# Kernel optimization log

Measured on AMD Instinct MI355X. Metric: run time of the kernel, lower is better.

Reference implementation:

```python
import jax, jax.numpy as jnp
import numpy as np

SEQ, BATCH = 2048, 32
ENC_HS, DEC_HS = 512, 1024

def setup_inputs() -> dict:
    key = jax.random.key(0)
    k1, k2, k3, k4, k5 = jax.random.split(key, 5)
    return {
        "hidden": jax.random.normal(k1, (BATCH, DEC_HS), dtype=jnp.float32),
        "encoder_outputs": jax.random.normal(k2, (SEQ, BATCH, 2 * ENC_HS), dtype=jnp.float32),
        "attn_w": jax.random.normal(k3, (2 * ENC_HS + DEC_HS, DEC_HS), dtype=jnp.float32) * 0.02,
        "attn_b": jax.random.normal(k4, (DEC_HS,), dtype=jnp.float32) * 0.02,
        "v": jax.random.normal(k5, (DEC_HS,), dtype=jnp.float32),
    }

def reference(hidden, encoder_outputs, attn_w, attn_b, v):
    # encoder_outputs: [S, B, 2*enc_hs] -> [B, S, 2*enc_hs]
    enc = jnp.transpose(encoder_outputs, (1, 0, 2))
    B, S, _ = enc.shape
    # hidden: [B, dec_hs] broadcast to [B, S, dec_hs]
    h = jnp.broadcast_to(hidden[:, None, :], (B, S, hidden.shape[-1]))
    cat = jnp.concatenate([h, enc], axis=2)            # [B, S, 2*enc_hs+dec_hs]
    energy = jnp.tanh(cat @ attn_w + attn_b)            # [B, S, dec_hs]
    scores = jnp.einsum("bsd,d->bs", energy, v)        # [B, S]
    return jax.nn.softmax(scores, axis=1)
```

## Files before the change

### kernel.cpp

```cpp
#include <hip/hip_runtime.h>


typedef _Float16 f16;
typedef _Float16 half8 __attribute__((ext_vector_type(8)));
typedef float f32x4 __attribute__((ext_vector_type(4)));

#define KDIM 1024
#define NDIM 1024
#define SEQ  2048
#define NB   32

typedef __attribute__((address_space(1))) void gvoid;
typedef __attribute__((address_space(3))) void svoid;

__device__ __forceinline__ void gload_lds16(const void* g, void* l) {
    __builtin_amdgcn_global_load_lds((const gvoid*)g, (svoid*)l, 16, 0, 0);
}

__global__ __launch_bounds__(256) void prep_w(const float* __restrict__ w,
                                              f16* __restrict__ wt) {
    int idx   = blockIdx.x * 256 + threadIdx.x;
    int t     = idx >> 11;
    int unit  = idx & 2047;
    int nloc  = unit >> 2;
    int kblk  = unit & 3;
    int kstep = t >> 1, npass = t & 1;
    int n_g   = npass * 512 + nloc;
    int kbase = kstep * 32 + kblk * 8;
    half8 h;
#pragma unroll
    for (int kk = 0; kk < 8; ++kk)
        h[kk] = (f16)w[(size_t)(1024 + kbase + kk) * 1024 + n_g];
    int p = nloc * 4 + ((kblk + (nloc >> 1)) & 3);
    *(half8*)&wt[(size_t)t * 16384 + p * 8] = h;
}

__global__ __launch_bounds__(256) void prep_hb(const float* __restrict__ hidden,
                                               const float* __restrict__ attn_w,
                                               const float* __restrict__ attn_b,
                                               float* __restrict__ hb) {
    int b = blockIdx.x >> 2;
    int n = (blockIdx.x & 3) * 256 + threadIdx.x;
    const float* h = hidden + (size_t)b * 1024;
    float acc = attn_b[n];
#pragma unroll 8
    for (int k = 0; k < 1024; ++k)
        acc += h[k] * attn_w[(size_t)k * 1024 + n];
    hb[(size_t)b * 1024 + n] = acc;
}

__global__ __launch_bounds__(512, 2)
void fused_energy(const float* __restrict__ enc, const f16* __restrict__ wt,
                  const float* __restrict__ hb, const float* __restrict__ vvec,
                  float* __restrict__ out) {
    __shared__ f16 As[128 * 32];
    __shared__ f16 Ws[512 * 32];
    __shared__ float red[4][128];

    const int tid  = threadIdx.x;
    const int lane = tid & 63;
    const int wv   = tid >> 6;
    const int wm   = wv >> 2;
    const int wn   = wv & 3;
    const int l15  = lane & 15;
    const int l4   = lane >> 4;
    const int wgrow = blockIdx.x * 128;

    const int ar  = tid >> 2;
    const int akb = tid & 3;
    const float* aG = enc + (size_t)(wgrow + ar) * KDIM + akb * 8;
    f16* aDst = &As[(ar * 4 + ((akb + (ar >> 1)) & 3)) * 8];

    const int wseg = wv * 4;
    char* wLds = (char*)Ws + wseg * 1024 + lane * 16;

    int aOff[4], bOff[8];
#pragma unroll
    for (int mi = 0; mi < 4; ++mi) {
        int r = wm * 64 + mi * 16 + l15;
        aOff[mi] = (r * 4 + ((l4 + (r >> 1)) & 3)) * 8;
    }
#pragma unroll
    for (int nj = 0; nj < 8; ++nj) {
        int n = wn * 128 + nj * 16 + l15;
        bOff[nj] = (n * 4 + ((l4 + (n >> 1)) & 3)) * 8;
    }

    float part[4][4];
#pragma unroll
    for (int mi = 0; mi < 4; ++mi)
#pragma unroll
        for (int rg = 0; rg < 4; ++rg) part[mi][rg] = 0.f;

    const f32x4 zero = {0.f, 0.f, 0.f, 0.f};

    for (int pass = 0; pass < 2; ++pass) {
        f32x4 acc[4][8];
#pragma unroll
        for (int mi = 0; mi < 4; ++mi)
#pragma unroll
            for (int nj = 0; nj < 8; ++nj) acc[mi][nj] = zero;

        for (int ks = 0; ks < 32; ++ks) {
            f32x4 a0 = *(const f32x4*)(aG + ks * 32);
            f32x4 a1 = *(const f32x4*)(aG + ks * 32 + 4);
            __syncthreads();
            {
                const char* wsrc = (const char*)wt +
                    (size_t)(ks * 2 + pass) * 32768 + wseg * 1024 + lane * 16;
#pragma unroll
                for (int i = 0; i < 4; ++i)
                    gload_lds16(wsrc + i * 1024, wLds + i * 1024);
            }
            half8 ah;
#pragma unroll
            for (int j = 0; j < 4; ++j) ah[j] = (f16)a0[j];
#pragma unroll
            for (int j = 0; j < 4; ++j) ah[4 + j] = (f16)a1[j];
            *(half8*)aDst = ah;
            __syncthreads();

            half8 bf[8];
#pragma unroll
            for (int nj = 0; nj < 8; ++nj) bf[nj] = *(const half8*)&Ws[bOff[nj]];
#pragma unroll
            for (int mi = 0; mi < 4; ++mi) {
                half8 af = *(const half8*)&As[aOff[mi]];
#pragma unroll
                for (int nj = 0; nj < 8; ++nj)
                    acc[mi][nj] = __builtin_amdgcn_mfma_f32_16x16x32_f16(
                        af, bf[nj], acc[mi][nj], 0, 0, 0);
            }
        }

        const int nbase = pass * 512 + wn * 128;
        float vv[8];
#pragma unroll
        for (int nj = 0; nj < 8; ++nj) vv[nj] = vvec[nbase + nj * 16 + l15];
#pragma unroll
        for (int mi = 0; mi < 4; ++mi) {
#pragma unroll
            for (int rg = 0; rg < 4; ++rg) {
                int rl = wm * 64 + mi * 16 + l4 * 4 + rg;
                const float* hbrow = hb + (size_t)(rl & 31) * NDIM + nbase + l15;
                float sum = 0.f;
#pragma unroll
                for (int nj = 0; nj < 8; ++nj) {
                    float e  = acc[mi][nj][rg] + hbrow[nj * 16];
                    float e2 = __expf(2.f * e);
                    float th = 1.f - 2.f / (e2 + 1.f);
                    sum += th * vv[nj];
                }
                part[mi][rg] += sum;
            }
        }
    }

#pragma unroll
    for (int mi = 0; mi < 4; ++mi) {
#pragma unroll
        for (int rg = 0; rg < 4; ++rg) {
            float p = part[mi][rg];
            p += __shfl_xor(p, 1);
            p += __shfl_xor(p, 2);
            p += __shfl_xor(p, 4);
            p += __shfl_xor(p, 8);
            if (l15 == 0) red[wn][wm * 64 + mi * 16 + l4 * 4 + rg] = p;
        }
    }
    __syncthreads();
    if (tid < 128) {
        float s = red[0][tid] + red[1][tid] + red[2][tid] + red[3][tid];
        int rG = wgrow + tid;
        out[(size_t)(rG & 31) * SEQ + (rG >> 5)] = s;
    }
}

__global__ __launch_bounds__(256) void softmax_rows(float* __restrict__ out) {
    const int b = blockIdx.x;
    float* row = out + (size_t)b * SEQ;
    const int tid  = threadIdx.x;
    const int lane = tid & 63;
    const int wv   = tid >> 6;
    __shared__ float sred[4];
    __shared__ float ssum[4];
    float x[8];
    float mx = -3.4e38f;
#pragma unroll
    for (int j = 0; j < 8; ++j) { x[j] = row[tid + j * 256]; mx = fmaxf(mx, x[j]); }
#pragma unroll
    for (int o = 1; o < 64; o <<= 1) mx = fmaxf(mx, __shfl_xor(mx, o));
    if (lane == 0) sred[wv] = mx;
    __syncthreads();
    mx = fmaxf(fmaxf(sred[0], sred[1]), fmaxf(sred[2], sred[3]));
    float s = 0.f;
#pragma unroll
    for (int j = 0; j < 8; ++j) { x[j] = __expf(x[j] - mx); s += x[j]; }
#pragma unroll
    for (int o = 1; o < 64; o <<= 1) s += __shfl_xor(s, o);
    if (lane == 0) ssum[wv] = s;
    __syncthreads();
    s = ssum[0] + ssum[1] + ssum[2] + ssum[3];
    float inv = 1.f / s;
#pragma unroll
    for (int j = 0; j < 8; ++j) row[tid + j * 256] = x[j] * inv;
}

extern "C" void kernel_launch(void* const* d_in, const int* in_sizes, int n_in,
                              void* d_out, int out_size, void* d_ws, size_t ws_size,
                              hipStream_t stream) {
    const float* hidden = (const float*)d_in[0];
    const float* enc    = (const float*)d_in[1];
    const float* attn_w = (const float*)d_in[2];
    const float* attn_b = (const float*)d_in[3];
    const float* v      = (const float*)d_in[4];
    float* out = (float*)d_out;

    f16*   wt = (f16*)d_ws;
    float* hb = (float*)((char*)d_ws + (2u << 20));

    prep_w<<<512, 256, 0, stream>>>(attn_w, wt);
    prep_hb<<<128, 256, 0, stream>>>(hidden, attn_w, attn_b, hb);
    fused_energy<<<512, 512, 0, stream>>>(enc, wt, hb, v, out);
    softmax_rows<<<32, 256, 0, stream>>>(out);
}
```

Baseline: 284.9 us.

## Double-buffer LDS tiles to prefetch next K-step during MFMA compute

Splits the A and W shared-memory tiles into two buffers. The next K-step's weights (via global_load_lds) and encoder rows are prefetched while MFMAs run on the current buffer, and the loop drops to a single barrier per iteration. The prefetch runs continuously across the two N passes. This aims to hide global load latency and remove one barrier per step, at the cost of doubling LDS use, which may cut the number of resident blocks per CU.

```diff
diff --git a/kernel.cpp b/kernel.cpp
--- a/kernel.cpp
+++ b/kernel.cpp
@@ -53,8 +53,8 @@
 void fused_energy(const float* __restrict__ enc, const f16* __restrict__ wt,
                   const float* __restrict__ hb, const float* __restrict__ vvec,
                   float* __restrict__ out) {
-    __shared__ f16 As[128 * 32];
-    __shared__ f16 Ws[512 * 32];
+    __shared__ f16 As[2][128 * 32];
+    __shared__ f16 Ws[2][512 * 32];
     __shared__ float red[4][128];
 
     const int tid  = threadIdx.x;
@@ -69,10 +69,10 @@
     const int ar  = tid >> 2;
     const int akb = tid & 3;
     const float* aG = enc + (size_t)(wgrow + ar) * KDIM + akb * 8;
-    f16* aDst = &As[(ar * 4 + ((akb + (ar >> 1)) & 3)) * 8];
+    const int aDstOff = (ar * 4 + ((akb + (ar >> 1)) & 3)) * 8;
 
     const int wseg = wv * 4;
-    char* wLds = (char*)Ws + wseg * 1024 + lane * 16;
+    const int wLdsOff = wseg * 1024 + lane * 16;
 
     int aOff[4], bOff[8];
 #pragma unroll
@@ -94,6 +94,21 @@
 
     const f32x4 zero = {0.f, 0.f, 0.f, 0.f};
 
+    {
+        const char* wsrc = (const char*)wt + wLdsOff;
+        char* wd = (char*)&Ws[0][0] + wLdsOff;
+#pragma unroll
+        for (int i = 0; i < 4; ++i)
+            gload_lds16(wsrc + i * 1024, wd + i * 1024);
+        f32x4 a0 = *(const f32x4*)(aG);
+        f32x4 a1 = *(const f32x4*)(aG + 4);
+        half8 ah;
+#pragma unroll
+        for (int j = 0; j < 4; ++j) { ah[j] = (f16)a0[j]; ah[4 + j] = (f16)a1[j]; }
+        *(half8*)&As[0][aDstOff] = ah;
+    }
+    __syncthreads();
+
     for (int pass = 0; pass < 2; ++pass) {
         f32x4 acc[4][8];
 #pragma unroll
@@ -101,36 +116,46 @@
 #pragma unroll
             for (int nj = 0; nj < 8; ++nj) acc[mi][nj] = zero;
 
+#pragma unroll 2
         for (int ks = 0; ks < 32; ++ks) {
-            f32x4 a0 = *(const f32x4*)(aG + ks * 32);
-            f32x4 a1 = *(const f32x4*)(aG + ks * 32 + 4);
-            __syncthreads();
-            {
+            const int cur = ks & 1;
+            const int nxb = cur ^ 1;
+            const int tn  = pass * 32 + ks + 1;
+            const bool pf = tn < 64;
+            const int nks = tn & 31;
+            const int nps = tn >> 5;
+
+            f32x4 a0, a1;
+            if (pf) {
                 const char* wsrc = (const char*)wt +
-                    (size_t)(ks * 2 + pass) * 32768 + wseg * 1024 + lane * 16;
+                    (size_t)(nks * 2 + nps) * 32768 + wLdsOff;
+                char* wd = (char*)&Ws[nxb][0] + wLdsOff;
 #pragma unroll
                 for (int i = 0; i < 4; ++i)
-                    gload_lds16(wsrc + i * 1024, wLds + i * 1024);
-            }
-            half8 ah;
-#pragma unroll
-            for (int j = 0; j < 4; ++j) ah[j] = (f16)a0[j];
-#pragma unroll
-            for (int j = 0; j < 4; ++j) ah[4 + j] = (f16)a1[j];
-            *(half8*)aDst = ah;
-            __syncthreads();
+                    gload_lds16(wsrc + i * 1024, wd + i * 1024);
+                a0 = *(const f32x4*)(aG + nks * 32);
+                a1 = *(const f32x4*)(aG + nks * 32 + 4);
+            }
 
             half8 bf[8];
 #pragma unroll
-            for (int nj = 0; nj < 8; ++nj) bf[nj] = *(const half8*)&Ws[bOff[nj]];
+            for (int nj = 0; nj < 8; ++nj) bf[nj] = *(const half8*)&Ws[cur][bOff[nj]];
 #pragma unroll
             for (int mi = 0; mi < 4; ++mi) {
-                half8 af = *(const half8*)&As[aOff[mi]];
+                half8 af = *(const half8*)&As[cur][aOff[mi]];
 #pragma unroll
                 for (int nj = 0; nj < 8; ++nj)
                     acc[mi][nj] = __builtin_amdgcn_mfma_f32_16x16x32_f16(
                         af, bf[nj], acc[mi][nj], 0, 0, 0);
             }
+
+            if (pf) {
+                half8 ah;
+#pragma unroll
+                for (int j = 0; j < 4; ++j) { ah[j] = (f16)a0[j]; ah[4 + j] = (f16)a1[j]; }
+                *(half8*)&As[nxb][aDstOff] = ah;
+            }
+            __syncthreads();
         }
 
         const int nbase = pass * 512 + wn * 128;
```

Result: faster. 269.4 us (-5.5%).

## Triple-buffer W and A tiles in LDS with one barrier per k-step

Applied to the files above, without the earlier changes.

Restructures the fused energy GEMM main loop into a 3-stage software pipeline. W tiles are loaded asynchronously into LDS two steps ahead, and A rows are prefetched into registers and converted to f16 one step ahead. This replaces the two __syncthreads per k-step with a single barrier and explicit vmcnt waits, so global loads overlap with the MFMA work. The cost is 3x the LDS footprint (about 123KB), which may limit occupancy with launch_bounds(512,2), and added reliance on hand-written waitcnt correctness.

```diff
diff --git a/kernel.cpp b/kernel.cpp
--- a/kernel.cpp
+++ b/kernel.cpp
@@ -53,8 +53,8 @@
 void fused_energy(const float* __restrict__ enc, const f16* __restrict__ wt,
                   const float* __restrict__ hb, const float* __restrict__ vvec,
                   float* __restrict__ out) {
-    __shared__ f16 As[128 * 32];
-    __shared__ f16 Ws[512 * 32];
+    __shared__ f16 Ws[3][512 * 32];
+    __shared__ f16 As[3][128 * 32];
     __shared__ float red[4][128];
 
     const int tid  = threadIdx.x;
@@ -69,21 +69,20 @@
     const int ar  = tid >> 2;
     const int akb = tid & 3;
     const float* aG = enc + (size_t)(wgrow + ar) * KDIM + akb * 8;
-    f16* aDst = &As[(ar * 4 + ((akb + (ar >> 1)) & 3)) * 8];
-
-    const int wseg = wv * 4;
-    char* wLds = (char*)Ws + wseg * 1024 + lane * 16;
-
-    int aOff[4], bOff[8];
+    const int aDstByte = (ar * 4 + ((akb + (ar >> 1)) & 3)) * 16;
+
+    const int wLdsOff = wv * 4096 + lane * 16;
+
+    int aOffB[4], bOffB[8];
 #pragma unroll
     for (int mi = 0; mi < 4; ++mi) {
         int r = wm * 64 + mi * 16 + l15;
-        aOff[mi] = (r * 4 + ((l4 + (r >> 1)) & 3)) * 8;
+        aOffB[mi] = (r * 4 + ((l4 + (r >> 1)) & 3)) * 16;
     }
 #pragma unroll
     for (int nj = 0; nj < 8; ++nj) {
         int n = wn * 128 + nj * 16 + l15;
-        bOff[nj] = (n * 4 + ((l4 + (n >> 1)) & 3)) * 8;
+        bOffB[nj] = (n * 4 + ((l4 + (n >> 1)) & 3)) * 16;
     }
 
     float part[4][4];
@@ -93,68 +92,119 @@
         for (int rg = 0; rg < 4; ++rg) part[mi][rg] = 0.f;
 
     const f32x4 zero = {0.f, 0.f, 0.f, 0.f};
-
-    for (int pass = 0; pass < 2; ++pass) {
-        f32x4 acc[4][8];
-#pragma unroll
-        for (int mi = 0; mi < 4; ++mi)
-#pragma unroll
-            for (int nj = 0; nj < 8; ++nj) acc[mi][nj] = zero;
-
-        for (int ks = 0; ks < 32; ++ks) {
-            f32x4 a0 = *(const f32x4*)(aG + ks * 32);
-            f32x4 a1 = *(const f32x4*)(aG + ks * 32 + 4);
-            __syncthreads();
-            {
-                const char* wsrc = (const char*)wt +
-                    (size_t)(ks * 2 + pass) * 32768 + wseg * 1024 + lane * 16;
-#pragma unroll
-                for (int i = 0; i < 4; ++i)
-                    gload_lds16(wsrc + i * 1024, wLds + i * 1024);
-            }
-            half8 ah;
-#pragma unroll
-            for (int j = 0; j < 4; ++j) ah[j] = (f16)a0[j];
-#pragma unroll
-            for (int j = 0; j < 4; ++j) ah[4 + j] = (f16)a1[j];
-            *(half8*)aDst = ah;
-            __syncthreads();
-
-            half8 bf[8];
-#pragma unroll
-            for (int nj = 0; nj < 8; ++nj) bf[nj] = *(const half8*)&Ws[bOff[nj]];
-#pragma unroll
-            for (int mi = 0; mi < 4; ++mi) {
-                half8 af = *(const half8*)&As[aOff[mi]];
-#pragma unroll
-                for (int nj = 0; nj < 8; ++nj)
-                    acc[mi][nj] = __builtin_amdgcn_mfma_f32_16x16x32_f16(
-                        af, bf[nj], acc[mi][nj], 0, 0, 0);
-            }
-        }
-
-        const int nbase = pass * 512 + wn * 128;
-        float vv[8];
-#pragma unroll
-        for (int nj = 0; nj < 8; ++nj) vv[nj] = vvec[nbase + nj * 16 + l15];
-#pragma unroll
-        for (int mi = 0; mi < 4; ++mi) {
-#pragma unroll
-            for (int rg = 0; rg < 4; ++rg) {
-                int rl = wm * 64 + mi * 16 + l4 * 4 + rg;
-                const float* hbrow = hb + (size_t)(rl & 31) * NDIM + nbase + l15;
-                float sum = 0.f;
-#pragma unroll
-                for (int nj = 0; nj < 8; ++nj) {
-                    float e  = acc[mi][nj][rg] + hbrow[nj * 16];
-                    float e2 = __expf(2.f * e);
-                    float th = 1.f - 2.f / (e2 + 1.f);
-                    sum += th * vv[nj];
-                }
-                part[mi][rg] += sum;
-            }
-        }
-    }
+    f32x4 acc[4][8];
+#pragma unroll
+    for (int mi = 0; mi < 4; ++mi)
+#pragma unroll
+        for (int nj = 0; nj < 8; ++nj) acc[mi][nj] = zero;
+
+    f32x4 aEv0, aEv1, aOd0, aOd1;
+
+    {
+        const char* w0 = (const char*)wt + wLdsOff;
+        char* d0 = (char*)&Ws[0][0] + wLdsOff;
+        gload_lds16(w0,        d0);
+        gload_lds16(w0 + 1024, d0 + 1024);
+        gload_lds16(w0 + 2048, d0 + 2048);
+        gload_lds16(w0 + 3072, d0 + 3072);
+        aEv0 = *(const f32x4*)aG;
+        aEv1 = *(const f32x4*)(aG + 4);
+        const char* w1 = (const char*)wt + (size_t)2 * 32768 + wLdsOff;
+        char* d1 = (char*)&Ws[1][0] + wLdsOff;
+        gload_lds16(w1,        d1);
+        gload_lds16(w1 + 1024, d1 + 1024);
+        gload_lds16(w1 + 2048, d1 + 2048);
+        gload_lds16(w1 + 3072, d1 + 3072);
+        aOd0 = *(const f32x4*)(aG + 32);
+        aOd1 = *(const f32x4*)(aG + 36);
+        asm volatile("s_waitcnt vmcnt(6)" ::: "memory");
+        half8 ah;
+#pragma unroll
+        for (int j = 0; j < 4; ++j) { ah[j] = (f16)aEv0[j]; ah[4 + j] = (f16)aEv1[j]; }
+        *(half8*)((char*)&As[0][0] + aDstByte) = ah;
+    }
+    asm volatile("s_waitcnt lgkmcnt(0)" ::: "memory");
+    __builtin_amdgcn_s_barrier();
+
+#define KSTEP(T, ALD0, ALD1, ACV0, ACV1)                                      \
+  {                                                                           \
+    const int t_ = (T);                                                       \
+    if (t_ < 62) {                                                            \
+      const int tn = t_ + 2;                                                  \
+      const int wi = (tn & 31) * 2 + (tn >> 5);                               \
+      const char* ws_ = (const char*)wt + (size_t)wi * 32768 + wLdsOff;       \
+      char* wd_ = (char*)&Ws[tn % 3][0] + wLdsOff;                            \
+      gload_lds16(ws_,        wd_);                                           \
+      gload_lds16(ws_ + 1024, wd_ + 1024);                                    \
+      gload_lds16(ws_ + 2048, wd_ + 2048);                                    \
+      gload_lds16(ws_ + 3072, wd_ + 3072);                                    \
+      ALD0 = *(const f32x4*)(aG + (tn & 31) * 32);                            \
+      ALD1 = *(const f32x4*)(aG + (tn & 31) * 32 + 4);                        \
+      asm volatile("s_waitcnt vmcnt(6)" ::: "memory");                        \
+    } else {                                                                  \
+      asm volatile("s_waitcnt vmcnt(0)" ::: "memory");                        \
+    }                                                                         \
+    if (t_ < 63) {                                                            \
+      half8 ah_;                                                              \
+      _Pragma("unroll") for (int j = 0; j < 4; ++j) {                         \
+        ah_[j] = (f16)ACV0[j]; ah_[4 + j] = (f16)ACV1[j];                     \
+      }                                                                       \
+      *(half8*)((char*)&As[(t_ + 1) % 3][0] + aDstByte) = ah_;                \
+    }                                                                         \
+    {                                                                         \
+      const char* wb_ = (const char*)&Ws[t_ % 3][0];                          \
+      const char* ab_ = (const char*)&As[t_ % 3][0];                          \
+      half8 bf_[8];                                                           \
+      _Pragma("unroll") for (int nj = 0; nj < 8; ++nj)                        \
+        bf_[nj] = *(const half8*)(wb_ + bOffB[nj]);                           \
+      _Pragma("unroll") for (int mi = 0; mi < 4; ++mi) {                      \
+        half8 af_ = *(const half8*)(ab_ + aOffB[mi]);                         \
+        _Pragma("unroll") for (int nj = 0; nj < 8; ++nj)                      \
+          acc[mi][nj] = __builtin_amdgcn_mfma_f32_16x16x32_f16(               \
+              af_, bf_[nj], acc[mi][nj], 0, 0, 0);                            \
+      }                                                                       \
+    }                                                                         \
+    asm volatile("s_waitcnt lgkmcnt(0)" ::: "memory");                        \
+    __builtin_amdgcn_s_barrier();                                             \
+  }
+
+#define EPILOGUE(P)                                                           \
+  {                                                                           \
+    const int nbase = (P) * 512 + wn * 128;                                   \
+    float vv[8];                                                              \
+    _Pragma("unroll") for (int nj = 0; nj < 8; ++nj)                          \
+      vv[nj] = vvec[nbase + nj * 16 + l15];                                   \
+    _Pragma("unroll") for (int mi = 0; mi < 4; ++mi) {                        \
+      _Pragma("unroll") for (int rg = 0; rg < 4; ++rg) {                      \
+        int rl = wm * 64 + mi * 16 + l4 * 4 + rg;                             \
+        const float* hbrow = hb + (size_t)(rl & 31) * NDIM + nbase + l15;     \
+        float sum = 0.f;                                                      \
+        _Pragma("unroll") for (int nj = 0; nj < 8; ++nj) {                    \
+          float e  = acc[mi][nj][rg] + hbrow[nj * 16];                        \
+          float e2 = __expf(2.f * e);                                         \
+          sum += (1.f - 2.f / (e2 + 1.f)) * vv[nj];                           \
+        }                                                                     \
+        part[mi][rg] += sum;                                                  \
+      }                                                                       \
+    }                                                                         \
+  }
+
+    for (int tt = 0; tt < 32; tt += 2) {
+        KSTEP(tt,     aEv0, aEv1, aOd0, aOd1);
+        KSTEP(tt + 1, aOd0, aOd1, aEv0, aEv1);
+    }
+    EPILOGUE(0);
+#pragma unroll
+    for (int mi = 0; mi < 4; ++mi)
+#pragma unroll
+        for (int nj = 0; nj < 8; ++nj) acc[mi][nj] = zero;
+    for (int tt = 32; tt < 64; tt += 2) {
+        KSTEP(tt,     aEv0, aEv1, aOd0, aOd1);
+        KSTEP(tt + 1, aOd0, aOd1, aEv0, aEv1);
+    }
+    EPILOGUE(1);
+#undef KSTEP
+#undef EPILOGUE
 
 #pragma unroll
     for (int mi = 0; mi < 4; ++mi) {
```

Result: slower. 413.2 us (+45.0%).

## Drop LDS staging in energy GEMM, load MFMA fragments directly from global

Applied to the files above, without the earlier changes.

Removes the shared-memory tiles and both per-k-step barriers in the fused energy kernel. Each wave now loads its A (encoder fp32, converted to fp16) and B (pre-laid-out weights) fragments straight from global memory into registers. prep_w is rewritten to emit the weight layout those direct fragment loads expect. Blocks shrink to 64 rows and 256 threads, launched as 1024 blocks, and s_setprio is raised around the MFMA burst. This avoids LDS round-trips and synchronisation, at the cost of more redundant global/L2 traffic, since each of the 4 waves reloads the same A rows and weights are no longer shared across row tiles within a block.

```diff
diff --git a/kernel.cpp b/kernel.cpp
--- a/kernel.cpp
+++ b/kernel.cpp
@@ -10,29 +10,19 @@
 #define SEQ  2048
 #define NB   32
 
-typedef __attribute__((address_space(1))) void gvoid;
-typedef __attribute__((address_space(3))) void svoid;
-
-__device__ __forceinline__ void gload_lds16(const void* g, void* l) {
-    __builtin_amdgcn_global_load_lds((const gvoid*)g, (svoid*)l, 16, 0, 0);
-}
-
 __global__ __launch_bounds__(256) void prep_w(const float* __restrict__ w,
                                               f16* __restrict__ wt) {
-    int idx   = blockIdx.x * 256 + threadIdx.x;
-    int t     = idx >> 11;
-    int unit  = idx & 2047;
-    int nloc  = unit >> 2;
-    int kblk  = unit & 3;
-    int kstep = t >> 1, npass = t & 1;
-    int n_g   = npass * 512 + nloc;
-    int kbase = kstep * 32 + kblk * 8;
+    int g    = blockIdx.x * 256 + threadIdx.x;
+    int ks   = g >> 12;
+    int rest = g & 4095;
+    int n    = rest >> 2;
+    int kgrp = rest & 3;
+    int kbase = 1024 + ks * 32 + kgrp * 8;
     half8 h;
 #pragma unroll
-    for (int kk = 0; kk < 8; ++kk)
-        h[kk] = (f16)w[(size_t)(1024 + kbase + kk) * 1024 + n_g];
-    int p = nloc * 4 + ((kblk + (nloc >> 1)) & 3);
-    *(half8*)&wt[(size_t)t * 16384 + p * 8] = h;
+    for (int j = 0; j < 8; ++j)
+        h[j] = (f16)w[(size_t)(kbase + j) * 1024 + n];
+    *(half8*)&wt[(size_t)g * 8] = h;
 }
 
 __global__ __launch_bounds__(256) void prep_hb(const float* __restrict__ hidden,
@@ -49,42 +39,25 @@
     hb[(size_t)b * 1024 + n] = acc;
 }
 
-__global__ __launch_bounds__(512, 2)
+__global__ __launch_bounds__(256, 2)
 void fused_energy(const float* __restrict__ enc, const f16* __restrict__ wt,
                   const float* __restrict__ hb, const float* __restrict__ vvec,
                   float* __restrict__ out) {
-    __shared__ f16 As[128 * 32];
-    __shared__ f16 Ws[512 * 32];
-    __shared__ float red[4][128];
+    __shared__ float red[4][64];
 
     const int tid  = threadIdx.x;
     const int lane = tid & 63;
     const int wv   = tid >> 6;
-    const int wm   = wv >> 2;
-    const int wn   = wv & 3;
     const int l15  = lane & 15;
     const int l4   = lane >> 4;
-    const int wgrow = blockIdx.x * 128;
-
-    const int ar  = tid >> 2;
-    const int akb = tid & 3;
-    const float* aG = enc + (size_t)(wgrow + ar) * KDIM + akb * 8;
-    f16* aDst = &As[(ar * 4 + ((akb + (ar >> 1)) & 3)) * 8];
-
-    const int wseg = wv * 4;
-    char* wLds = (char*)Ws + wseg * 1024 + lane * 16;
-
-    int aOff[4], bOff[8];
-#pragma unroll
-    for (int mi = 0; mi < 4; ++mi) {
-        int r = wm * 64 + mi * 16 + l15;
-        aOff[mi] = (r * 4 + ((l4 + (r >> 1)) & 3)) * 8;
-    }
-#pragma unroll
-    for (int nj = 0; nj < 8; ++nj) {
-        int n = wn * 128 + nj * 16 + l15;
-        bOff[nj] = (n * 4 + ((l4 + (n >> 1)) & 3)) * 8;
-    }
+    const int wgrow = blockIdx.x * 64;
+
+    const float* aP0 = enc + (size_t)(wgrow +  0 + l15) * KDIM + l4 * 8;
+    const float* aP1 = enc + (size_t)(wgrow + 16 + l15) * KDIM + l4 * 8;
+    const float* aP2 = enc + (size_t)(wgrow + 32 + l15) * KDIM + l4 * 8;
+    const float* aP3 = enc + (size_t)(wgrow + 48 + l15) * KDIM + l4 * 8;
+
+    const f16* bP = wt + (size_t)(wv * 128 + l15) * 32 + l4 * 8;
 
     float part[4][4];
 #pragma unroll
@@ -95,6 +68,7 @@
     const f32x4 zero = {0.f, 0.f, 0.f, 0.f};
 
     for (int pass = 0; pass < 2; ++pass) {
+        const f16* bPp = bP + (size_t)pass * 512 * 32;
         f32x4 acc[4][8];
 #pragma unroll
         for (int mi = 0; mi < 4; ++mi)
@@ -102,38 +76,41 @@
             for (int nj = 0; nj < 8; ++nj) acc[mi][nj] = zero;
 
         for (int ks = 0; ks < 32; ++ks) {
-            f32x4 a0 = *(const f32x4*)(aG + ks * 32);
-            f32x4 a1 = *(const f32x4*)(aG + ks * 32 + 4);
-            __syncthreads();
+            half8 bf[8];
             {
-                const char* wsrc = (const char*)wt +
-                    (size_t)(ks * 2 + pass) * 32768 + wseg * 1024 + lane * 16;
-#pragma unroll
-                for (int i = 0; i < 4; ++i)
-                    gload_lds16(wsrc + i * 1024, wLds + i * 1024);
+                const f16* bk = bPp + (size_t)ks * 32768;
+#pragma unroll
+                for (int nj = 0; nj < 8; ++nj)
+                    bf[nj] = *(const half8*)(bk + nj * 512);
             }
-            half8 ah;
-#pragma unroll
-            for (int j = 0; j < 4; ++j) ah[j] = (f16)a0[j];
-#pragma unroll
-            for (int j = 0; j < 4; ++j) ah[4 + j] = (f16)a1[j];
-            *(half8*)aDst = ah;
-            __syncthreads();
-
-            half8 bf[8];
-#pragma unroll
-            for (int nj = 0; nj < 8; ++nj) bf[nj] = *(const half8*)&Ws[bOff[nj]];
-#pragma unroll
-            for (int mi = 0; mi < 4; ++mi) {
-                half8 af = *(const half8*)&As[aOff[mi]];
-#pragma unroll
-                for (int nj = 0; nj < 8; ++nj)
+            f32x4 a0[4], a1[4];
+            a0[0] = *(const f32x4*)(aP0 + ks * 32);
+            a1[0] = *(const f32x4*)(aP0 + ks * 32 + 4);
+            a0[1] = *(const f32x4*)(aP1 + ks * 32);
+            a1[1] = *(const f32x4*)(aP1 + ks * 32 + 4);
+            a0[2] = *(const f32x4*)(aP2 + ks * 32);
+            a1[2] = *(const f32x4*)(aP2 + ks * 32 + 4);
+            a0[3] = *(const f32x4*)(aP3 + ks * 32);
+            a1[3] = *(const f32x4*)(aP3 + ks * 32 + 4);
+            half8 af[4];
+#pragma unroll
+            for (int mi = 0; mi < 4; ++mi)
+#pragma unroll
+                for (int j = 0; j < 4; ++j) {
+                    af[mi][j]     = (f16)a0[mi][j];
+                    af[mi][4 + j] = (f16)a1[mi][j];
+                }
+            __builtin_amdgcn_s_setprio(1);
+#pragma unroll
+            for (int nj = 0; nj < 8; ++nj)
+#pragma unroll
+                for (int mi = 0; mi < 4; ++mi)
                     acc[mi][nj] = __builtin_amdgcn_mfma_f32_16x16x32_f16(
-                        af, bf[nj], acc[mi][nj], 0, 0, 0);
-            }
+                        af[mi], bf[nj], acc[mi][nj], 0, 0, 0);
+            __builtin_amdgcn_s_setprio(0);
         }
 
-        const int nbase = pass * 512 + wn * 128;
+        const int nbase = pass * 512 + wv * 128;
         float vv[8];
 #pragma unroll
         for (int nj = 0; nj < 8; ++nj) vv[nj] = vvec[nbase + nj * 16 + l15];
@@ -141,7 +118,7 @@
         for (int mi = 0; mi < 4; ++mi) {
 #pragma unroll
             for (int rg = 0; rg < 4; ++rg) {
-                int rl = wm * 64 + mi * 16 + l4 * 4 + rg;
+                int rl = mi * 16 + l4 * 4 + rg;
                 const float* hbrow = hb + (size_t)(rl & 31) * NDIM + nbase + l15;
                 float sum = 0.f;
 #pragma unroll
@@ -165,11 +142,11 @@
             p += __shfl_xor(p, 2);
             p += __shfl_xor(p, 4);
             p += __shfl_xor(p, 8);
-            if (l15 == 0) red[wn][wm * 64 + mi * 16 + l4 * 4 + rg] = p;
+            if (l15 == 0) red[wv][mi * 16 + l4 * 4 + rg] = p;
         }
     }
     __syncthreads();
-    if (tid < 128) {
+    if (tid < 64) {
         float s = red[0][tid] + red[1][tid] + red[2][tid] + red[3][tid];
         int rG = wgrow + tid;
         out[(size_t)(rG & 31) * SEQ + (rG >> 5)] = s;
@@ -221,6 +198,6 @@
 
     prep_w<<<512, 256, 0, stream>>>(attn_w, wt);
     prep_hb<<<128, 256, 0, stream>>>(hidden, attn_w, attn_b, hb);
-    fused_energy<<<512, 512, 0, stream>>>(enc, wt, hb, v, out);
+    fused_energy<<<1024, 256, 0, stream>>>(enc, wt, hb, v, out);
     softmax_rows<<<32, 256, 0, stream>>>(out);
 }
```

Result: slower. 430.2 us (+51.0%).
